# Kernel tuning notes

Hardware: AMD Instinct MI355X
Metric: run time of the kernel (lower is better)

The kernel has to match this reference:

```python
import jax, jax.numpy as jnp
import numpy as np

TOP_K = 2000
NUM_DETS = 1000
BASE_LAYER_RANGE = (24.0, 48.0, 24.0, 48.0)  # (min_y, max_y, min_x, max_x) from db.configs


def _topk(heat, K):
    # heat: [B, C, H, W] -> topk over flattened C*H*W (CornerNet-style)
    B, C, H, W = heat.shape
    scores, inds = jax.lax.top_k(heat.reshape(B, -1), K)
    clses = inds // (H * W)
    sp_inds = inds % (H * W)            # spatial index into H*W
    ys = (sp_inds // W).astype(heat.dtype)
    xs = (sp_inds % W).astype(heat.dtype)
    return scores, sp_inds, clses, ys, xs


def _transpose_and_gather(feat, ind):
    # feat: [B, C, H, W], ind: [B, K] spatial indices -> [B, K, C]
    B, C, H, W = feat.shape
    feat = feat.transpose(0, 2, 3, 1).reshape(B, H * W, C)
    return feat[jnp.arange(B)[:, None], ind]


def _gather_feat(feat, ind):
    # feat: [B, N, C], ind: [B, K] -> [B, K, C]
    B = feat.shape[0]
    return feat[jnp.arange(B)[:, None], ind]


def _decode_layer(heat, tl_regr, br_regr, H0, W0, layer_idx):
    B, C, H, W = heat.shape
    dt = heat.dtype
    height_scale = 8.0 * H0 / H
    width_scale = 8.0 * W0 / W
    K = min(TOP_K, H * W)
    scores, inds, clses, ys, xs = _topk(heat, K)
    ys = ys.reshape(B, K, 1)
    xs = xs.reshape(B, K, 1)
    tlr = _transpose_and_gather(tl_regr, inds).reshape(B, K, 1, 2)
    brr = _transpose_and_gather(br_regr, inds).reshape(B, K, 1, 2)
    min_y, max_y, min_x, max_x = [v / 8.0 / 2.0 for v in BASE_LAYER_RANGE]
    tl_xs = xs - ((max_x - min_x) * tlr[..., 0] + (max_x + min_x) / 2.0)
    tl_ys = ys - ((max_y - min_y) * tlr[..., 1] + (max_y + min_y) / 2.0)
    br_xs = xs + ((max_x - min_x) * brr[..., 0] + (max_x + min_x) / 2.0)
    br_ys = ys + ((max_y - min_y) * brr[..., 1] + (max_y + min_y) / 2.0)
    bboxes = jnp.stack((tl_xs, tl_ys, br_xs, br_ys), axis=3)  # [B, K, 1, 4]
    sc = scores.reshape(B, K, 1)
    invalid = (br_xs < tl_xs) | (br_ys < tl_ys)
    sc = jnp.where(invalid, jnp.asarray(-1.0, dt), sc)
    sc = sc.reshape(B, -1)
    nd = min(NUM_DETS, sc.shape[1])
    sc, top = jax.lax.top_k(sc, nd)
    sc = sc[:, :, None]
    bboxes = _gather_feat(bboxes.reshape(B, -1, 4), top)
    bboxes = bboxes * jnp.asarray([width_scale, height_scale, width_scale, height_scale], dt)
    # layer_detections: zeros [B, nd, 7]; [:,:,:5] = cat([scores, bboxes]); then row 6 set to i
    det = jnp.concatenate([sc, bboxes, jnp.zeros((B, nd, 2), dt)], axis=2)
    det = det.at[:, 6, :].set(jnp.asarray(float(layer_idx), dt))  # faithful to `[:, 6] = i`
    return det


def setup_inputs() -> dict:
    key = jax.random.key(0)
    ks = jax.random.split(key, 9)
    B, C = 16, 80
    sizes = [(128, 128), (64, 64), (32, 32)]
    inp = {}
    for i, (H, W) in enumerate(sizes):
        inp[f"heat{i}"] = jax.random.uniform(ks[3 * i], (B, C, H, W), dtype=jnp.float32)
        inp[f"tl{i}"] = jax.random.normal(ks[3 * i + 1], (B, 2, H, W), dtype=jnp.float32)
        inp[f"br{i}"] = jax.random.normal(ks[3 * i + 2], (B, 2, H, W), dtype=jnp.float32)
    return inp


def reference(heat0, heat1, heat2, tl0, tl1, tl2, br0, br1, br2):
    heats = [heat0, heat1, heat2]
    tls = [tl0, tl1, tl2]
    brs = [br0, br1, br2]
    _, _, H0, W0 = heats[0].shape
    dets = [_decode_layer(heats[i], tls[i], brs[i], H0, W0, i) for i in range(3)]
    detections = jnp.concatenate(dets, axis=1)  # [B, sum_nd, 7]
    nd = min(NUM_DETS, detections.shape[1])
    _, top = jax.lax.top_k(detections[:, :, 0], nd)
    return _gather_feat(detections, top)
```

## Files before the change

kernel.cpp:

```cpp
#include <hip/hip_runtime.h>


#define NB 1024
#define CHUNK 32768

__device__ __forceinline__ unsigned int ord_f32(float f) {
    unsigned int b = __float_as_uint(f);
    return (b & 0x80000000u) ? ~b : (b | 0x80000000u);
}
__device__ __forceinline__ float unord_f32(unsigned int o) {
    unsigned int b = (o & 0x80000000u) ? (o & 0x7fffffffu) : ~o;
    return __uint_as_float(b);
}
__device__ __forceinline__ int bucket_of(float f) {
    int bi = (int)(f * (float)NB);
    bi = bi < 0 ? 0 : (bi > NB - 1 ? NB - 1 : bi);
    return bi;
}

__device__ __forceinline__ int layer_N(int l)   { return (l == 0) ? 1310720 : (l == 1) ? 327680 : 81920; }
__device__ __forceinline__ int nchunks(int l)   { return (l == 0) ? 40 : (l == 1) ? 10 : 3; }
__device__ __forceinline__ int chunk_base(int l){ return (l == 0) ? 0 : (l == 1) ? 640 : 800; }
__device__ __forceinline__ float TL_of(int l)   { return (l == 0) ? 0.998046875f : (l == 1) ? 0.9921875f : 0.98125f; }
__device__ __forceinline__ int seg_cap(int l)   { return (l == 0) ? 256 : (l == 1) ? 768 : 1024; }
__device__ __forceinline__ int loose_base(int l){ return (l == 0) ? 0 : (l == 1) ? 163840 : 286720; }

__global__ __launch_bounds__(256) void collect_kernel(
    const float* __restrict__ h0, const float* __restrict__ h1, const float* __restrict__ h2,
    int* __restrict__ pbc, unsigned long long* __restrict__ loose)
{
    int l = blockIdx.z, b = blockIdx.y, chunk = blockIdx.x;
    int nc = nchunks(l);
    if (chunk >= nc) return;
    int N = layer_N(l);
    int elems = min(CHUNK, N - chunk * CHUNK);
    const float* heat = (l == 0) ? h0 : (l == 1) ? h1 : h2;
    float TL = TL_of(l);

    __shared__ int lc;
    __shared__ unsigned long long lbuf[1024];
    if (threadIdx.x == 0) lc = 0;
    __syncthreads();

    const float4* p = (const float4*)(heat + (size_t)b * N + (size_t)chunk * CHUNK);
    int base = chunk * CHUNK;
    int n4 = elems >> 2;
    for (int i = threadIdx.x; i < n4; i += 256) {
        float4 v = p[i];
        float vs[4] = {v.x, v.y, v.z, v.w};
#pragma unroll
        for (int cc = 0; cc < 4; cc++) {
            if (vs[cc] >= TL) {
                int pos = atomicAdd(&lc, 1);
                if (pos < 1024) {
                    unsigned int idx = (unsigned int)(base + 4 * i + cc);
                    lbuf[pos] = ((unsigned long long)ord_f32(vs[cc]) << 32) | (unsigned int)(~idx);
                }
            }
        }
    }
    __syncthreads();
    int pidx = chunk_base(l) + b * nc + chunk;
    if (threadIdx.x == 0) pbc[pidx] = lc;
    int cap = seg_cap(l);
    int n = min(lc, cap);
    unsigned long long* seg = loose + loose_base(l) + (size_t)(b * nc + chunk) * cap;
    for (int i = threadIdx.x; i < n; i += 256) seg[i] = lbuf[i];
}

__device__ __forceinline__ unsigned long long shfl_xor_u64(unsigned long long a, int j) {
    unsigned int lo = (unsigned int)a, hi = (unsigned int)(a >> 32);
    lo = (unsigned int)__shfl_xor((int)lo, j, 64);
    hi = (unsigned int)__shfl_xor((int)hi, j, 64);
    return ((unsigned long long)hi << 32) | lo;
}

template<int K, int J>
struct PhaseH {
    static __device__ __forceinline__ void run(unsigned long long (&v)[8], int lane) {
        constexpr int JR = J >> 6;
#pragma unroll
        for (int r = 0; r < 8; r++) {
            if ((r & JR) == 0) {
                int i = (r << 6) | lane;
                unsigned long long a = v[r], bb = v[r | JR];
                bool sw = ((i & K) == 0) ? (a < bb) : (a > bb);
                if (sw) { v[r] = bb; v[r | JR] = a; }
            }
        }
        PhaseH<K, (J >> 1)>::run(v, lane);
    }
};

template<int K>
struct PhaseH<K, 32> {
    static __device__ __forceinline__ void run(unsigned long long (&v)[8], int lane) {
#pragma unroll
        for (int js = 32; js >= 1; js >>= 1) {
            if (K > js) {
#pragma unroll
                for (int r = 0; r < 8; r++) {
                    unsigned long long a = v[r];
                    unsigned long long w = shfl_xor_u64(a, js);
                    int i = (r << 6) | lane;
                    bool upper = (lane & js) != 0;
                    bool keep_max = (((i & K) == 0) != upper);
                    bool agw = a > w;
                    v[r] = (keep_max == agw) ? a : w;
                }
            }
        }
    }
};

template<int K>
struct StageH {
    static __device__ __forceinline__ void run(unsigned long long (&v)[8], int lane) {
        PhaseH<K, (K > 64 ? (K >> 1) : 32)>::run(v, lane);
        StageH<(K << 1)>::run(v, lane);
    }
};
template<>
struct StageH<1024> {
    static __device__ __forceinline__ void run(unsigned long long (&)[8], int) {}
};

__global__ __launch_bounds__(512) void sort_kernel(
    const float* __restrict__ h0, const float* __restrict__ h1, const float* __restrict__ h2,
    const int* __restrict__ pbc, const unsigned long long* __restrict__ loose,
    unsigned long long* __restrict__ cand)
{
    int bl = blockIdx.x;
    int l = bl >> 4, b = bl & 15;
    int K = (l == 2) ? 1024 : 2000;
    int nc = nchunks(l);
    int cap = seg_cap(l);
    int tid = threadIdx.x;
    int lane = tid & 63;
    int wid = tid >> 6;

    __shared__ unsigned long long A[4096];
    __shared__ unsigned long long Bq[4096];
    __shared__ int offs[41];
    __shared__ int s_bad, s_tot;

    if (tid == 0) {
        int o = 0, bad = 0;
        const int* pb = pbc + chunk_base(l) + b * nc;
        for (int c = 0; c < nc; c++) {
            int raw = pb[c];
            if (raw > cap) bad = 1;
            offs[c] = o;
            o += min(raw, cap);
        }
        offs[nc] = o;
        if (o < K || o > 4096) bad = 1;
        s_bad = bad;
        s_tot = o;
    }
    __syncthreads();

    if (!s_bad) {
        const unsigned long long* lb = loose + loose_base(l) + (size_t)b * nc * cap;
        for (int c = 0; c < nc; c++) {
            int o = offs[c], n_c = offs[c + 1] - o;
            const unsigned long long* sg = lb + (size_t)c * cap;
            for (int i = tid; i < n_c; i += 512) A[o + i] = sg[i];
        }
        for (int i = s_tot + tid; i < 4096; i += 512) A[i] = (unsigned long long)i;
    } else {
        __shared__ int lh[NB];
        __shared__ int st, lc2;
        for (int i = tid; i < NB; i += 512) lh[i] = 0;
        if (tid == 0) lc2 = 0;
        __syncthreads();
        int N = layer_N(l);
        const float* hp = ((l == 0) ? h0 : (l == 1) ? h1 : h2) + (size_t)b * N;
        for (int i = tid; i < N; i += 512) atomicAdd(&lh[bucket_of(hp[i])], 1);
        __syncthreads();
        if (tid == 0) {
            int acc = 0, bidx;
            for (bidx = NB - 1; bidx > 0; bidx--) {
                acc += lh[bidx];
                if (acc >= K) break;
            }
            st = bidx;
        }
        __syncthreads();
        int t = st;
        for (int i = tid; i < N; i += 512) {
            float x = hp[i];
            if (bucket_of(x) >= t) {
                int pos = atomicAdd(&lc2, 1);
                if (pos < 4096)
                    A[pos] = ((unsigned long long)ord_f32(x) << 32) | (unsigned int)(~(unsigned int)i);
            }
        }
        __syncthreads();
        for (int i = min(lc2, 4096) + tid; i < 4096; i += 512) A[i] = (unsigned long long)i;
    }
    __syncthreads();

    int base = wid << 9;
    unsigned long long v[8];
#pragma unroll
    for (int r = 0; r < 8; r++) v[r] = A[base | (r << 6) | lane];

    StageH<2>::run(v, lane);

#pragma unroll
    for (int r = 0; r < 8; r++) A[base | (r << 6) | lane] = v[r];
    __syncthreads();

#pragma unroll
    for (int r = 0; r < 8; r++) {
        unsigned long long key = v[r];
        int lo[7];
#pragma unroll
        for (int q = 0; q < 7; q++) lo[q] = 0;
#pragma unroll
        for (int h = 256; h >= 1; h >>= 1) {
#pragma unroll
            for (int q = 0; q < 7; q++) {
                int w2 = q + (q >= wid ? 1 : 0);
                unsigned long long p = A[(w2 << 9) + lo[q] + h - 1];
                lo[q] += (p > key) ? h : 0;
            }
        }
        int rank = (r << 6) | lane;
#pragma unroll
        for (int q = 0; q < 7; q++) {
            int w2 = q + (q >= wid ? 1 : 0);
            unsigned long long p = A[(w2 << 9) + lo[q]];
            rank += lo[q] + ((p > key) ? 1 : 0);
        }
        Bq[rank] = key;
    }
    __syncthreads();

    unsigned long long* cd = cand + (size_t)bl * 4096;
    for (int i = tid; i < 4096; i += 512) cd[i] = Bq[i];
}

__global__ __launch_bounds__(1024) void build_kernel(
    const float* __restrict__ t0, const float* __restrict__ t1, const float* __restrict__ t2,
    const float* __restrict__ r0, const float* __restrict__ r1, const float* __restrict__ r2,
    const unsigned long long* __restrict__ cand, float* __restrict__ det)
{
    int l = blockIdx.x >> 4;
    int b = blockIdx.x & 15;
    int bl = l * 16 + b;
    int HW = (l == 0) ? 16384 : (l == 1) ? 4096 : 1024;
    int W  = (l == 0) ? 128 : (l == 1) ? 64 : 32;
    int K  = (l == 2) ? 1024 : 2000;
    float scale = (l == 0) ? 8.f : (l == 1) ? 16.f : 32.f;
    const float* tlp = (l == 0) ? t0 : (l == 1) ? t1 : t2;
    const float* brp = (l == 0) ? r0 : (l == 1) ? r1 : r2;

    const unsigned long long* srt = cand + (size_t)bl * 4096;

    __shared__ int wsum[16];
    int tid = threadIdx.x;
    int lane = tid & 63, wid = tid >> 6;

    float s_[2], bx_[2][4];
    int f_[2];
#pragma unroll
    for (int q = 0; q < 2; q++) {
        int k = 2 * tid + q;
        f_[q] = 0;
        if (k < K) {
            unsigned long long kk = srt[k];
            unsigned int idx = ~(unsigned int)kk;
            float score = unord_f32((unsigned int)(kk >> 32));
            int sp = (int)(idx % (unsigned)HW);
            float xs = (float)(sp % W), ys = (float)(sp / W);
            float tv0 = tlp[((size_t)b * 2 + 0) * HW + sp];
            float tv1 = tlp[((size_t)b * 2 + 1) * HW + sp];
            float bv0 = brp[((size_t)b * 2 + 0) * HW + sp];
            float bv1 = brp[((size_t)b * 2 + 1) * HW + sp];
            float tlx = __fsub_rn(xs, __fadd_rn(__fmul_rn(1.5f, tv0), 2.25f));
            float tly = __fsub_rn(ys, __fadd_rn(__fmul_rn(1.5f, tv1), 2.25f));
            float brx = __fadd_rn(xs, __fadd_rn(__fmul_rn(1.5f, bv0), 2.25f));
            float bry = __fadd_rn(ys, __fadd_rn(__fmul_rn(1.5f, bv1), 2.25f));
            bool invalid = (brx < tlx) || (bry < tly);
            f_[q] = invalid ? 0 : 1;
            s_[q] = invalid ? -1.0f : score;
            bx_[q][0] = __fmul_rn(tlx, scale);
            bx_[q][1] = __fmul_rn(tly, scale);
            bx_[q][2] = __fmul_rn(brx, scale);
            bx_[q][3] = __fmul_rn(bry, scale);
        }
    }
    int mysum = f_[0] + f_[1];

    int x = mysum;
#pragma unroll
    for (int off = 1; off < 64; off <<= 1) {
        int y = __shfl_up(x, off, 64);
        if (lane >= off) x += y;
    }
    if (lane == 63) wsum[wid] = x;
    __syncthreads();
    if (wid == 0 && lane < 16) {
        int s = wsum[lane];
#pragma unroll
        for (int off = 1; off < 16; off <<= 1) {
            int y = __shfl_up(s, off, 64);
            if (lane >= off) s += y;
        }
        wsum[lane] = s;
    }
    __syncthreads();
    int wave_off = (wid > 0) ? wsum[wid - 1] : 0;
    int V = wsum[15];
    int base_excl = (x + wave_off) - mysum;

    float* dbase = det + ((size_t)b * 3000 + (size_t)l * 1000) * 7;
#pragma unroll
    for (int q = 0; q < 2; q++) {
        int k = 2 * tid + q;
        if (k < K) {
            int pos = base_excl + (q == 1 ? f_[0] : 0);
            int rank = f_[q] ? pos : V + (k - pos);
            if (rank < 1000 && rank != 6) {
                float* drow = dbase + (size_t)rank * 7;
                drow[0] = s_[q];
                drow[1] = bx_[q][0];
                drow[2] = bx_[q][1];
                drow[3] = bx_[q][2];
                drow[4] = bx_[q][3];
                drow[5] = 0.f;
                drow[6] = 0.f;
            }
        }
    }
    if (tid == 0) {
        float lv = (float)l;
        float* drow = dbase + 6 * 7;
#pragma unroll
        for (int j = 0; j < 7; j++) drow[j] = lv;
    }
}

__device__ __forceinline__ bool key_gt(float sa, int ga, float sb, int gb) {
    return (sa > sb) || (sa == sb && ga < gb);
}

__global__ __launch_bounds__(1024) void final_kernel(const float* __restrict__ det,
                                                     float* __restrict__ out)
{
    int b = blockIdx.x;
    __shared__ float sc[3000];
    int tid = threadIdx.x;
    const float* dbase = det + (size_t)b * 3000 * 7;
    for (int i = tid; i < 3000; i += 1024) sc[i] = dbase[(size_t)i * 7];
    __syncthreads();

    for (int e = tid; e < 3000; e += 1024) {
        float se = sc[e];
        int ge = e;
        int rank = 0;
#pragma unroll
        for (int lp = 0; lp < 3; lp++) {
            int lo = 0, hiB = 999;
            while (lo < hiB) {
                int mid = (lo + hiB) >> 1;
                int p = mid + (mid >= 6 ? 1 : 0);
                int g = lp * 1000 + p;
                if (key_gt(sc[g], g, se, ge)) lo = mid + 1; else hiB = mid;
            }
            rank += lo;
        }
#pragma unroll
        for (int ls = 0; ls < 3; ls++) {
            int g = ls * 1000 + 6;
            if (g != e && key_gt((float)ls, g, se, ge)) rank++;
        }
        if (rank < 1000) {
            const float* src = dbase + (size_t)e * 7;
            float* dst = out + ((size_t)b * 1000 + rank) * 7;
#pragma unroll
            for (int j = 0; j < 7; j++) dst[j] = src[j];
        }
    }
}

extern "C" void kernel_launch(void* const* d_in, const int* in_sizes, int n_in,
                              void* d_out, int out_size, void* d_ws, size_t ws_size,
                              hipStream_t stream)
{
    (void)in_sizes; (void)n_in; (void)out_size; (void)ws_size;
    const float* h0 = (const float*)d_in[0];
    const float* t0 = (const float*)d_in[1];
    const float* r0 = (const float*)d_in[2];
    const float* h1 = (const float*)d_in[3];
    const float* t1 = (const float*)d_in[4];
    const float* r1 = (const float*)d_in[5];
    const float* h2 = (const float*)d_in[6];
    const float* t2 = (const float*)d_in[7];
    const float* r2 = (const float*)d_in[8];
    float* out = (float*)d_out;

    char* ws = (char*)d_ws;
    int* pbc  = (int*)ws;
    unsigned long long* loose = (unsigned long long*)(ws + 3392);
    unsigned long long* cand  = (unsigned long long*)(ws + 2690368);
    float* det = (float*)(ws + 4263232);

    collect_kernel<<<dim3(40, 16, 3), 256, 0, stream>>>(h0, h1, h2, pbc, loose);
    sort_kernel<<<48, 512, 0, stream>>>(h0, h1, h2, pbc, loose, cand);
    build_kernel<<<48, 1024, 0, stream>>>(t0, t1, t2, r0, r1, r2, cand, det);
    final_kernel<<<16, 1024, 0, stream>>>(det, out);
}
```

Before: 243.6 us.

## Split sort into per-wave bitonic kernel and parallel merge-rank kernel

The single 48-block sort kernel becomes two kernels. The first runs 384 one-wave blocks, each bitonic-sorting a 512-element sublist in registers after gathering candidates directly from the loose segments. The second uses a 48x4 grid, where each block ranks 1024 keys against the other sorted sublists by binary search and scatters them straight to global memory. The aim is to spread the sort across many more CUs than the original 48 blocks, at the cost of an extra launch and a global round-trip for the sublists. The fallback path now uses a shared-memory bitonic sort.

```diff
diff --git a/kernel.cpp b/kernel.cpp
--- a/kernel.cpp
+++ b/kernel.cpp
@@ -125,50 +125,128 @@
     static __device__ __forceinline__ void run(unsigned long long (&)[8], int) {}
 };
 
-__global__ __launch_bounds__(512) void sort_kernel(
-    const float* __restrict__ h0, const float* __restrict__ h1, const float* __restrict__ h2,
+__global__ __launch_bounds__(64) void sortA_kernel(
     const int* __restrict__ pbc, const unsigned long long* __restrict__ loose,
-    unsigned long long* __restrict__ cand)
-{
-    int bl = blockIdx.x;
+    unsigned long long* __restrict__ subl, int* __restrict__ badf)
+{
+    int bx = blockIdx.x;
+    int bl = bx >> 3, w = bx & 7;
     int l = bl >> 4, b = bl & 15;
     int K = (l == 2) ? 1024 : 2000;
     int nc = nchunks(l);
     int cap = seg_cap(l);
+    int lane = threadIdx.x;
+
+    __shared__ int offs[64];
+
+    int raw = 0;
+    if (lane < nc) raw = pbc[chunk_base(l) + b * nc + lane];
+    int cnt_c = min(raw, cap);
+    bool ovf = (lane < nc) && (raw > cap);
+    unsigned long long ovfmask = __ballot(ovf);
+    int x = cnt_c;
+#pragma unroll
+    for (int off = 1; off < 64; off <<= 1) {
+        int y = __shfl_up(x, off, 64);
+        if (lane >= off) x += y;
+    }
+    int tot = __shfl(x, 63, 64);
+
+    offs[lane] = 0x7fffffff;
+    __syncthreads();
+    if (lane < nc) offs[lane + 1] = x;
+    if (lane == 0) offs[0] = 0;
+    __syncthreads();
+
+    bool bad = (ovfmask != 0ull) || (tot < K) || (tot > 4096);
+    if (lane == 0) badf[bl] = bad ? 1 : 0;
+    if (bad) return;
+
+    const unsigned long long* lb = loose + loose_base(l) + (size_t)b * nc * cap;
+    unsigned long long v[8];
+#pragma unroll
+    for (int r = 0; r < 8; r++) {
+        int g = (w << 9) | (r << 6) | lane;
+        unsigned long long key;
+        if (g >= tot) {
+            key = (unsigned long long)g;
+        } else {
+            int c = 0, oc = 0;
+#pragma unroll
+            for (int step = 32; step >= 1; step >>= 1) {
+                int cc = c + step;
+                int ov = offs[cc];
+                if (ov <= g) { c = cc; oc = ov; }
+            }
+            key = lb[(size_t)c * cap + (g - oc)];
+        }
+        v[r] = key;
+    }
+
+    StageH<2>::run(v, lane);
+
+    unsigned long long* dst = subl + (size_t)bl * 4096 + (w << 9);
+#pragma unroll
+    for (int r = 0; r < 8; r++) dst[(r << 6) | lane] = v[r];
+}
+
+__device__ void bitonic_desc(unsigned long long* d, int n, int tid, int nt) {
+    for (int k = 2; k <= n; k <<= 1) {
+        for (int j = k >> 1; j > 0; j >>= 1) {
+            __syncthreads();
+            for (int i = tid; i < n; i += nt) {
+                int ixj = i ^ j;
+                if (ixj > i) {
+                    unsigned long long a = d[i], bb = d[ixj];
+                    bool sw = ((i & k) == 0) ? (a < bb) : (a > bb);
+                    if (sw) { d[i] = bb; d[ixj] = a; }
+                }
+            }
+        }
+    }
+    __syncthreads();
+}
+
+__global__ __launch_bounds__(512) void sortB_kernel(
+    const float* __restrict__ h0, const float* __restrict__ h1, const float* __restrict__ h2,
+    const int* __restrict__ pbc, const unsigned long long* __restrict__ loose,
+    const int* __restrict__ badf, const unsigned long long* __restrict__ subl,
+    unsigned long long* __restrict__ cand)
+{
+    int bl = blockIdx.x;
+    int part = blockIdx.y;
+    int l = bl >> 4, b = bl & 15;
+    int K = (l == 2) ? 1024 : 2000;
     int tid = threadIdx.x;
-    int lane = tid & 63;
-    int wid = tid >> 6;
 
     __shared__ unsigned long long A[4096];
-    __shared__ unsigned long long Bq[4096];
-    __shared__ int offs[41];
-    __shared__ int s_bad, s_tot;
-
-    if (tid == 0) {
-        int o = 0, bad = 0;
-        const int* pb = pbc + chunk_base(l) + b * nc;
-        for (int c = 0; c < nc; c++) {
-            int raw = pb[c];
-            if (raw > cap) bad = 1;
-            offs[c] = o;
-            o += min(raw, cap);
-        }
-        offs[nc] = o;
-        if (o < K || o > 4096) bad = 1;
-        s_bad = bad;
-        s_tot = o;
-    }
-    __syncthreads();
-
-    if (!s_bad) {
-        const unsigned long long* lb = loose + loose_base(l) + (size_t)b * nc * cap;
-        for (int c = 0; c < nc; c++) {
-            int o = offs[c], n_c = offs[c + 1] - o;
-            const unsigned long long* sg = lb + (size_t)c * cap;
-            for (int i = tid; i < n_c; i += 512) A[o + i] = sg[i];
-        }
-        for (int i = s_tot + tid; i < 4096; i += 512) A[i] = (unsigned long long)i;
+    unsigned long long* cd = cand + (size_t)bl * 4096;
+
+    if (!badf[bl]) {
+        const unsigned long long* sl = subl + (size_t)bl * 4096;
+        for (int i = tid; i < 4096; i += 512) A[i] = sl[i];
+        __syncthreads();
+
+#pragma unroll
+        for (int e0 = 0; e0 < 2; e0++) {
+            int wsrc = (part << 1) | e0;
+            unsigned long long key = A[(wsrc << 9) | tid];
+            int rank = tid;
+#pragma unroll
+            for (int q = 0; q < 7; q++) {
+                int w2 = q + (q >= wsrc ? 1 : 0);
+                int lo = 0;
+                for (int h = 256; h >= 1; h >>= 1) {
+                    unsigned long long p = A[(w2 << 9) + lo + h - 1];
+                    lo += (p > key) ? h : 0;
+                }
+                unsigned long long p = A[(w2 << 9) + lo];
+                rank += lo + ((p > key) ? 1 : 0);
+            }
+            cd[rank] = key;
+        }
     } else {
+        if (part != 0) return;
         __shared__ int lh[NB];
         __shared__ int st, lc2;
         for (int i = tid; i < NB; i += 512) lh[i] = 0;
@@ -189,57 +267,18 @@
         __syncthreads();
         int t = st;
         for (int i = tid; i < N; i += 512) {
-            float x = hp[i];
-            if (bucket_of(x) >= t) {
+            float xx = hp[i];
+            if (bucket_of(xx) >= t) {
                 int pos = atomicAdd(&lc2, 1);
                 if (pos < 4096)
-                    A[pos] = ((unsigned long long)ord_f32(x) << 32) | (unsigned int)(~(unsigned int)i);
+                    A[pos] = ((unsigned long long)ord_f32(xx) << 32) | (unsigned int)(~(unsigned int)i);
             }
         }
         __syncthreads();
         for (int i = min(lc2, 4096) + tid; i < 4096; i += 512) A[i] = (unsigned long long)i;
-    }
-    __syncthreads();
-
-    int base = wid << 9;
-    unsigned long long v[8];
-#pragma unroll
-    for (int r = 0; r < 8; r++) v[r] = A[base | (r << 6) | lane];
-
-    StageH<2>::run(v, lane);
-
-#pragma unroll
-    for (int r = 0; r < 8; r++) A[base | (r << 6) | lane] = v[r];
-    __syncthreads();
-
-#pragma unroll
-    for (int r = 0; r < 8; r++) {
-        unsigned long long key = v[r];
-        int lo[7];
-#pragma unroll
-        for (int q = 0; q < 7; q++) lo[q] = 0;
-#pragma unroll
-        for (int h = 256; h >= 1; h >>= 1) {
-#pragma unroll
-            for (int q = 0; q < 7; q++) {
-                int w2 = q + (q >= wid ? 1 : 0);
-                unsigned long long p = A[(w2 << 9) + lo[q] + h - 1];
-                lo[q] += (p > key) ? h : 0;
-            }
-        }
-        int rank = (r << 6) | lane;
-#pragma unroll
-        for (int q = 0; q < 7; q++) {
-            int w2 = q + (q >= wid ? 1 : 0);
-            unsigned long long p = A[(w2 << 9) + lo[q]];
-            rank += lo[q] + ((p > key) ? 1 : 0);
-        }
-        Bq[rank] = key;
-    }
-    __syncthreads();
-
-    unsigned long long* cd = cand + (size_t)bl * 4096;
-    for (int i = tid; i < 4096; i += 512) cd[i] = Bq[i];
+        bitonic_desc(A, 4096, tid, 512);
+        for (int i = tid; i < 4096; i += 512) cd[i] = A[i];
+    }
 }
 
 __global__ __launch_bounds__(1024) void build_kernel(
@@ -404,12 +443,15 @@
 
     char* ws = (char*)d_ws;
     int* pbc  = (int*)ws;
-    unsigned long long* loose = (unsigned long long*)(ws + 3392);
-    unsigned long long* cand  = (unsigned long long*)(ws + 2690368);
-    float* det = (float*)(ws + 4263232);
+    int* badf = (int*)(ws + 3392);
+    unsigned long long* loose = (unsigned long long*)(ws + 3584);
+    unsigned long long* subl  = (unsigned long long*)(ws + 2690560);
+    unsigned long long* cand  = (unsigned long long*)(ws + 4263424);
+    float* det = (float*)(ws + 5836288);
 
     collect_kernel<<<dim3(40, 16, 3), 256, 0, stream>>>(h0, h1, h2, pbc, loose);
-    sort_kernel<<<48, 512, 0, stream>>>(h0, h1, h2, pbc, loose, cand);
+    sortA_kernel<<<384, 64, 0, stream>>>(pbc, loose, subl, badf);
+    sortB_kernel<<<dim3(48, 4), 512, 0, stream>>>(h0, h1, h2, pbc, loose, badf, subl, cand);
     build_kernel<<<48, 1024, 0, stream>>>(t0, t1, t2, r0, r1, r2, cand, det);
     final_kernel<<<16, 1024, 0, stream>>>(det, out);
 }
```

Result: faster. 216.3 us (-11.2%).
